# Optimization experiments

Measured on AMD Instinct MI355X. Metric: run time of the kernel, lower is better.

Reference implementation:

```python
import jax, jax.numpy as jnp
import numpy as np

B, T, E, C = 64, 512, 768, 20


def setup_inputs() -> dict:
    key = jax.random.key(0)
    ks = jax.random.split(key, 8)
    hidden = jax.random.normal(ks[0], (B, T, E), jnp.float32)
    attention_mask = jnp.ones((B, T), jnp.int32)
    labels = jax.random.randint(ks[1], (B, T), 0, C)
    fc_w = jax.random.normal(ks[2], (C, E), jnp.float32) * 0.02
    fc_b = jnp.zeros((C,), jnp.float32)
    # torchcrf initializes transitions ~ Uniform(-0.1, 0.1)
    start_transitions = jax.random.uniform(ks[3], (C,), jnp.float32, -0.1, 0.1)
    end_transitions = jax.random.uniform(ks[4], (C,), jnp.float32, -0.1, 0.1)
    transitions = jax.random.uniform(ks[5], (C, C), jnp.float32, -0.1, 0.1)
    return {"hidden": hidden, "attention_mask": attention_mask, "labels": labels,
            "fc_w": fc_w, "fc_b": fc_b, "start_transitions": start_transitions,
            "end_transitions": end_transitions, "transitions": transitions}


def _crf_log_likelihood(emissions, tags, mask, start_t, end_t, trans):
    # emissions [B,T,C], tags [B,T] int, mask [B,T]
    Bn = emissions.shape[0]
    emT = jnp.swapaxes(emissions, 0, 1)            # [T,B,C]
    tagsT = jnp.swapaxes(tags, 0, 1)               # [T,B]
    maskT = jnp.swapaxes(mask, 0, 1).astype(emissions.dtype)  # [T,B]
    barange = jnp.arange(Bn)
    # --- numerator: score of the gold path ---
    score = start_t[tagsT[0]] + emT[0, barange, tagsT[0]]
    def num_step(s, x):
        em_t, tag_t, tag_p, m_t = x
        s = s + (trans[tag_p, tag_t] + em_t[barange, tag_t]) * m_t
        return s, None
    score, _ = jax.lax.scan(num_step, score, (emT[1:], tagsT[1:], tagsT[:-1], maskT[1:]))
    seq_ends = jnp.sum(mask, axis=1).astype(jnp.int32) - 1
    last_tags = tags[barange, seq_ends]
    score = score + end_t[last_tags]
    # --- denominator: forward algorithm (logsumexp recurrence) ---
    alpha = start_t[None, :] + emT[0]              # [B,C]
    def den_step(a, x):
        em_t, m_t = x
        nxt = jax.nn.logsumexp(a[:, :, None] + trans[None, :, :] + em_t[:, None, :], axis=1)
        a = jnp.where(m_t[:, None] > 0, nxt, a)
        return a, None
    alpha, _ = jax.lax.scan(den_step, alpha, (emT[1:], maskT[1:]))
    norm = jax.nn.logsumexp(alpha + end_t[None, :], axis=1)
    return score - norm


def _viterbi_decode(emissions, mask, start_t, end_t, trans):
    emT = jnp.swapaxes(emissions, 0, 1)            # [T,B,C]
    maskT = jnp.swapaxes(mask, 0, 1)               # [T,B]
    alpha = start_t[None, :] + emT[0]              # [B,C]
    def step(a, x):
        em_t, m_t = x
        sc = a[:, :, None] + trans[None, :, :]     # [B, prev C, cur C]
        best = jnp.max(sc, axis=1) + em_t
        idx = jnp.argmax(sc, axis=1)               # [B,C] best prev tag
        a2 = jnp.where(m_t[:, None] > 0, best, a)
        return a2, idx
    alpha, hist = jax.lax.scan(step, alpha, (emT[1:], maskT[1:]))  # hist [T-1,B,C]
    last = jnp.argmax(alpha + end_t[None, :], axis=1)  # [B]
    def back(tag, idx_t):
        prev = jnp.take_along_axis(idx_t, tag[:, None], axis=1)[:, 0]
        return prev, prev
    _, prevs = jax.lax.scan(back, last, hist, reverse=True)  # [T-1,B]
    path = jnp.concatenate([jnp.swapaxes(prevs, 0, 1), last[:, None]], axis=1)  # [B,T]
    return path


def reference(hidden, attention_mask, labels, fc_w, fc_b, start_transitions, end_transitions, transitions):
    # linear head on BERT hidden states -> per-token emissions
    emissions = jnp.einsum('bte,ce->btc', hidden, fc_w) + fc_b
    llh = _crf_log_likelihood(emissions, labels, attention_mask,
                              start_transitions, end_transitions, transitions)
    loss = -jnp.mean(llh)  # crf(..., reduction='mean') negated
    path = _viterbi_decode(emissions, attention_mask, start_transitions,
                           end_transitions, transitions) + 1  # res_paths = x + 1
    return (loss, path)
```

## Files before the change

### kernel.cpp

```cpp
#include <hip/hip_runtime.h>
#include <hip/hip_bf16.h>

#define BB 64
#define TT 512
#define EE 768
#define CC 20
#define MID 256

typedef __attribute__((ext_vector_type(8))) short bf16x8;
typedef __attribute__((ext_vector_type(4))) float f32x4;

__device__ __forceinline__ float rlane(float x, int l) {
  return __int_as_float(__builtin_amdgcn_readlane(__float_as_int(x), l));
}
__device__ __forceinline__ short f2bf(float x) {
  union { __hip_bfloat16 h; short s; } u;
  u.h = __float2bfloat16(x);
  return u.s;
}
__device__ __forceinline__ bf16x8 pack8(float4 a, float4 b) {
  bf16x8 r;
  r[0] = f2bf(a.x); r[1] = f2bf(a.y); r[2] = f2bf(a.z); r[3] = f2bf(a.w);
  r[4] = f2bf(b.x); r[5] = f2bf(b.y); r[6] = f2bf(b.z); r[7] = f2bf(b.w);
  return r;
}

__global__ __launch_bounds__(256) void packw_kernel(const float* __restrict__ fc_w,
                                                    short* __restrict__ wfrag) {
  int t = blockIdx.x * 256 + threadIdx.x;
  int lane = t & 63;
  int kc = (t >> 6) % 24;
  int tile = t / (24 * 64);
  int n = tile * 16 + (lane & 15);
  if (n >= CC) n = CC - 1;
  int k0 = kc * 32 + (lane >> 4) * 8;
  const float* src = fc_w + (size_t)n * EE + k0;
  float4 x = *(const float4*)src;
  float4 y = *(const float4*)(src + 4);
  ((bf16x8*)wfrag)[t] = pack8(x, y);
}

__global__ __launch_bounds__(256) void emissions_kernel(
    const float* __restrict__ hidden, const short* __restrict__ wfrag,
    const float* __restrict__ fc_b, float* __restrict__ em) {
  const int wave = threadIdx.x >> 6;
  const int lane = threadIdx.x & 63;
  const int token0 = blockIdx.x * 64 + wave * 16;
  const int m = lane & 15, q = lane >> 4;
  const float* hrow = hidden + (size_t)(token0 + m) * EE + q * 8;
  const bf16x8* wp = (const bf16x8*)wfrag;
  f32x4 acc0 = {0.f, 0.f, 0.f, 0.f}, acc1 = {0.f, 0.f, 0.f, 0.f};
#pragma unroll 4
  for (int kb = 0; kb < 24; ++kb) {
    float4 a0 = *(const float4*)(hrow + kb * 32);
    float4 a1 = *(const float4*)(hrow + kb * 32 + 4);
    bf16x8 Ab = pack8(a0, a1);
    bf16x8 w0 = wp[kb * 64 + lane];
    bf16x8 w1 = wp[(24 + kb) * 64 + lane];
    acc0 = __builtin_amdgcn_mfma_f32_16x16x32_bf16(Ab, w0, acc0, 0, 0, 0);
    acc1 = __builtin_amdgcn_mfma_f32_16x16x32_bf16(Ab, w1, acc1, 0, 0, 0);
  }
  const int col = lane & 15;
  const float b0v = fc_b[col];
  const bool has1 = (16 + col < CC);
  const float b1v = has1 ? fc_b[16 + col] : 0.f;
#pragma unroll
  for (int r = 0; r < 4; ++r) {
    int tok = token0 + q * 4 + r;
    em[(size_t)tok * CC + col] = acc0[r] + b0v;
    if (has1) em[(size_t)tok * CC + 16 + col] = acc1[r] + b1v;
  }
}

__device__ __forceinline__ unsigned umax_(unsigned a, unsigned b) { return a > b ? a : b; }
__device__ __forceinline__ unsigned umax3_(unsigned a, unsigned b, unsigned c) {
  return umax_(umax_(a, b), c);
}
#define PDECL(Q) unsigned p##Q = (__float_as_uint(rlane(a, Q) + tv[Q]) & 0xFFFFFFE0u) | Q##u;
__device__ __forceinline__ void vstep(float a, const float (&tv)[CC], float& vm, int& jm) {
  PDECL(0) PDECL(1) PDECL(2) PDECL(3) PDECL(4) PDECL(5) PDECL(6) PDECL(7)
  PDECL(8) PDECL(9) PDECL(10) PDECL(11) PDECL(12) PDECL(13) PDECL(14)
  PDECL(15) PDECL(16) PDECL(17) PDECL(18) PDECL(19)
  unsigned m0 = umax3_(p0, p1, p2);
  unsigned m1 = umax3_(p3, p4, p5);
  unsigned m2 = umax3_(p6, p7, p8);
  unsigned m3 = umax3_(p9, p10, p11);
  unsigned m4 = umax3_(p12, p13, p14);
  unsigned m5 = umax3_(p15, p16, p17);
  unsigned n0 = umax3_(m0, m1, m2);
  unsigned n1 = umax3_(m3, m4, m5);
  unsigned n2 = umax_(p18, p19);
  unsigned r = umax3_(n0, n1, n2);
  vm = __uint_as_float(r & 0xFFFFFFE0u);
  jm = (int)(r & 31u);
}

#define XDECL(Q) float x##Q = rlane(x, Q); int y##Q = Q;
#define MRX(A_, B_) { bool k_ = (x##A_ >= x##B_); x##A_ = k_ ? x##A_ : x##B_; y##A_ = k_ ? y##A_ : y##B_; }
__device__ __forceinline__ int lane_argmax(float x) {
  XDECL(0) XDECL(1) XDECL(2) XDECL(3) XDECL(4) XDECL(5) XDECL(6) XDECL(7)
  XDECL(8) XDECL(9) XDECL(10) XDECL(11) XDECL(12) XDECL(13) XDECL(14)
  XDECL(15) XDECL(16) XDECL(17) XDECL(18) XDECL(19)
  MRX(0, 10) MRX(1, 11) MRX(2, 12) MRX(3, 13) MRX(4, 14)
  MRX(5, 15) MRX(6, 16) MRX(7, 17) MRX(8, 18) MRX(9, 19)
  MRX(0, 5) MRX(1, 6) MRX(2, 7) MRX(3, 8) MRX(4, 9)
  MRX(0, 1) MRX(2, 3)
  MRX(0, 2) MRX(0, 4)
  return y0;
}

__device__ __forceinline__ float fdot(float Es, const float (&ET)[CC]) {
  float s0 = rlane(Es, 0) * ET[0];
  float s1 = rlane(Es, 1) * ET[1];
  float s2 = rlane(Es, 2) * ET[2];
  float s3 = rlane(Es, 3) * ET[3];
  s0 = fmaf(rlane(Es, 4), ET[4], s0);
  s1 = fmaf(rlane(Es, 5), ET[5], s1);
  s2 = fmaf(rlane(Es, 6), ET[6], s2);
  s3 = fmaf(rlane(Es, 7), ET[7], s3);
  s0 = fmaf(rlane(Es, 8), ET[8], s0);
  s1 = fmaf(rlane(Es, 9), ET[9], s1);
  s2 = fmaf(rlane(Es, 10), ET[10], s2);
  s3 = fmaf(rlane(Es, 11), ET[11], s3);
  s0 = fmaf(rlane(Es, 12), ET[12], s0);
  s1 = fmaf(rlane(Es, 13), ET[13], s1);
  s2 = fmaf(rlane(Es, 14), ET[14], s2);
  s3 = fmaf(rlane(Es, 15), ET[15], s3);
  s0 = fmaf(rlane(Es, 16), ET[16], s0);
  s1 = fmaf(rlane(Es, 17), ET[17], s1);
  s2 = fmaf(rlane(Es, 18), ET[18], s2);
  s3 = fmaf(rlane(Es, 19), ET[19], s3);
  return (s0 + s1) + (s2 + s3);
}

__global__ __launch_bounds__(64) void crf_half_kernel(
    const float* __restrict__ em, const int* __restrict__ mask,
    const float* __restrict__ st, const float* __restrict__ en,
    const float* __restrict__ tr,
    float* __restrict__ amw, float* __restrict__ bmw,
    float* __restrict__ avw, float* __restrict__ bvw,
    unsigned char* __restrict__ bpws, unsigned char* __restrict__ fpws) {
  __shared__ float emsh[(MID + 1) * CC];
  __shared__ int msh[TT];
  const int tid = threadIdx.x;
  const int quad = blockIdx.x >> 6;
  const int b = blockIdx.x & (BB - 1);
  const int back = quad & 1;
  const int cc = tid < CC ? tid : CC - 1;
  const float K = 1.44269504088896340736f;
  const float BIAS = 64.0f;

  {
    const float* base = em + (size_t)b * TT * CC + (back ? MID * CC : 0);
    int nf4 = back ? (MID * CC / 4) : ((MID + 1) * CC / 4);
    const float4* src = (const float4*)base;
    float4* dst = (float4*)emsh;
    for (int i = tid; i < nf4; i += 64) dst[i] = src[i];
    for (int i = tid; i < TT; i += 64) msh[i] = mask[b * TT + i];
  }
  __syncthreads();

  if (quad == 0) {
    float ET[CC];
#pragma unroll
    for (int q = 0; q < CC; ++q) ET[q] = __builtin_amdgcn_exp2f(tr[q * CC + cc] * K);
    float r = st[cc] + emsh[cc];
    float base0 = rlane(r, 0);
    float Es = __builtin_amdgcn_exp2f((r - base0) * K);
    float off = base0 * K;
    int ie = 0;
    float emc = emsh[CC + cc];
    int mcur = msh[1];
    float eec = __builtin_amdgcn_exp2f(emc * K);
    for (int t = 1; t <= MID; ++t) {
      int tn = (t < MID) ? t + 1 : t;
      float emn = emsh[tn * CC + cc];
      int mn = msh[tn];
      float s = fdot(Es, ET) * eec;
      Es = mcur ? s : Es;
      if ((t & 7) == 0) {
        float p = rlane(Es, 0);
        int e = ((__float_as_int(p) >> 23) & 255) - 127;
        Es *= __int_as_float((127 - e) << 23);
        ie += e;
      }
      eec = __builtin_amdgcn_exp2f(emn * K);
      mcur = mn;
    }
    if (tid < CC) amw[b * CC + tid] = off + (float)ie + __builtin_amdgcn_logf(Es);
  } else if (quad == 1) {
    float ETr[CC];
#pragma unroll
    for (int q = 0; q < CC; ++q) ETr[q] = __builtin_amdgcn_exp2f(tr[cc * CC + q] * K);
    const float ENc = __builtin_amdgcn_exp2f(en[cc] * K);
    float Bs = ENc;
    int ie = 0;
    float em1 = emsh[(TT - 1 - MID) * CC + cc];
    int m1 = msh[TT - 1];
    float ee1 = __builtin_amdgcn_exp2f(em1 * K);
    for (int t = TT - 2; t >= MID; --t) {
      float emn = emsh[(t - MID) * CC + cc];
      int mn = msh[t];
      float G = Bs * ee1;
      float s = fdot(G, ETr);
      Bs = m1 ? s : ENc;
      ie = m1 ? ie : 0;
      if ((t & 7) == 0) {
        float p = rlane(Bs, 0);
        int e = ((__float_as_int(p) >> 23) & 255) - 127;
        Bs *= __int_as_float((127 - e) << 23);
        ie += e;
      }
      ee1 = __builtin_amdgcn_exp2f(emn * K);
      m1 = mn;
    }
    if (tid < CC) bmw[b * CC + tid] = (float)ie + __builtin_amdgcn_logf(Bs);
  } else if (quad == 2) {
    float tv[CC];
#pragma unroll
    for (int q = 0; q < CC; ++q) tv[q] = tr[q * CC + cc];
    float a = st[cc] + emsh[cc] + BIAS;
    float emc = emsh[CC + cc];
    int mcur = msh[1];
    unsigned char* bp = bpws + (size_t)b * MID * CC;
    for (int t = 1; t <= MID; ++t) {
      int tn = (t < MID) ? t + 1 : t;
      float emn = emsh[tn * CC + cc];
      int mn = msh[tn];
      float vm;
      int jm;
      vstep(a, tv, vm, jm);
      if (tid < CC) bp[(t - 1) * CC + tid] = (unsigned char)jm;
      float au = vm + emc;
      a = mcur ? au : a;
      if ((t & 7) == 0) a += (BIAS - rlane(a, 0));
      emc = emn;
      mcur = mn;
    }
    if (tid < CC) avw[b * CC + tid] = a;
  } else {
    float tv[CC];
#pragma unroll
    for (int q = 0; q < CC; ++q) tv[q] = tr[cc * CC + q];
    const float ENv = en[cc] + BIAS;
    float Vb = ENv;
    float em1 = emsh[(TT - 1 - MID) * CC + cc];
    int m1 = msh[TT - 1];
    unsigned char* fp = fpws + (size_t)b * MID * CC;
    for (int t = TT - 2; t >= MID; --t) {
      float emn = emsh[(t - MID) * CC + cc];
      int mn = msh[t];
      float a = Vb + em1;
      float vm;
      int jm;
      vstep(a, tv, vm, jm);
      if (tid < CC) fp[(t - MID) * CC + tid] = (unsigned char)jm;
      Vb = m1 ? vm : ENv;
      if ((t & 7) == 0) Vb += (BIAS - rlane(Vb, 0));
      em1 = emn;
      m1 = mn;
    }
    if (tid < CC) bvw[b * CC + tid] = Vb;
  }
}

__global__ __launch_bounds__(64) void finish_kernel(
    const float* __restrict__ em, const int* __restrict__ mask,
    const int* __restrict__ labels, const float* __restrict__ st,
    const float* __restrict__ en, const float* __restrict__ tr,
    const float* __restrict__ amw, const float* __restrict__ bmw,
    const float* __restrict__ avw, const float* __restrict__ bvw,
    const unsigned char* __restrict__ bpws, const unsigned char* __restrict__ fpws,
    float* __restrict__ llh, float* __restrict__ out) {
  __shared__ unsigned char hl[2 * MID * CC];
  const int b = blockIdx.x;
  const int tid = threadIdx.x;
  const int cc = tid < CC ? tid : CC - 1;
  const float LN2 = 0.69314718055994530942f;
  {
    const int4* bsrc = (const int4*)(bpws + (size_t)b * MID * CC);
    const int4* fsrc = (const int4*)(fpws + (size_t)b * MID * CC);
    int4* dst = (int4*)hl;
    for (int i = tid; i < 320; i += 64) {
      dst[i] = bsrc[i];
      dst[320 + i] = fsrc[i];
    }
  }
  __syncthreads();

  int cstar = lane_argmax(avw[b * CC + cc] + bvw[b * CC + cc]);
  float* ob = out + 1 + (size_t)b * TT;
  if (tid == 0) ob[MID] = (float)(cstar + 1);
  {
    int tag = cstar;
    int s = MID - 1;
    while (s >= 7) {
      int g0 = hl[(s - 0) * CC + cc];
      int g1 = hl[(s - 1) * CC + cc];
      int g2 = hl[(s - 2) * CC + cc];
      int g3 = hl[(s - 3) * CC + cc];
      int g4 = hl[(s - 4) * CC + cc];
      int g5 = hl[(s - 5) * CC + cc];
      int g6 = hl[(s - 6) * CC + cc];
      int g7 = hl[(s - 7) * CC + cc];
      tag = __builtin_amdgcn_readlane(g0, tag); float f0 = (float)(tag + 1);
      tag = __builtin_amdgcn_readlane(g1, tag); float f1 = (float)(tag + 1);
      tag = __builtin_amdgcn_readlane(g2, tag); float f2 = (float)(tag + 1);
      tag = __builtin_amdgcn_readlane(g3, tag); float f3 = (float)(tag + 1);
      tag = __builtin_amdgcn_readlane(g4, tag); float f4 = (float)(tag + 1);
      tag = __builtin_amdgcn_readlane(g5, tag); float f5 = (float)(tag + 1);
      tag = __builtin_amdgcn_readlane(g6, tag); float f6 = (float)(tag + 1);
      tag = __builtin_amdgcn_readlane(g7, tag); float f7 = (float)(tag + 1);
      if (tid == 0) {
        ob[s - 0] = f0; ob[s - 1] = f1; ob[s - 2] = f2; ob[s - 3] = f3;
        ob[s - 4] = f4; ob[s - 5] = f5; ob[s - 6] = f6; ob[s - 7] = f7;
      }
      s -= 8;
    }
  }
  {
    int tag = cstar;
    int u = 0;
    while (u + 7 <= MID - 2) {
      int g0 = hl[MID * CC + (u + 0) * CC + cc];
      int g1 = hl[MID * CC + (u + 1) * CC + cc];
      int g2 = hl[MID * CC + (u + 2) * CC + cc];
      int g3 = hl[MID * CC + (u + 3) * CC + cc];
      int g4 = hl[MID * CC + (u + 4) * CC + cc];
      int g5 = hl[MID * CC + (u + 5) * CC + cc];
      int g6 = hl[MID * CC + (u + 6) * CC + cc];
      int g7 = hl[MID * CC + (u + 7) * CC + cc];
      tag = __builtin_amdgcn_readlane(g0, tag); float f0 = (float)(tag + 1);
      tag = __builtin_amdgcn_readlane(g1, tag); float f1 = (float)(tag + 1);
      tag = __builtin_amdgcn_readlane(g2, tag); float f2 = (float)(tag + 1);
      tag = __builtin_amdgcn_readlane(g3, tag); float f3 = (float)(tag + 1);
      tag = __builtin_amdgcn_readlane(g4, tag); float f4 = (float)(tag + 1);
      tag = __builtin_amdgcn_readlane(g5, tag); float f5 = (float)(tag + 1);
      tag = __builtin_amdgcn_readlane(g6, tag); float f6 = (float)(tag + 1);
      tag = __builtin_amdgcn_readlane(g7, tag); float f7 = (float)(tag + 1);
      if (tid == 0) {
        ob[MID + 1 + u + 0] = f0; ob[MID + 1 + u + 1] = f1;
        ob[MID + 1 + u + 2] = f2; ob[MID + 1 + u + 3] = f3;
        ob[MID + 1 + u + 4] = f4; ob[MID + 1 + u + 5] = f5;
        ob[MID + 1 + u + 6] = f6; ob[MID + 1 + u + 7] = f7;
      }
      u += 8;
    }
    while (u <= MID - 2) {
      int g = hl[MID * CC + u * CC + cc];
      tag = __builtin_amdgcn_readlane(g, tag);
      if (tid == 0) ob[MID + 1 + u] = (float)(tag + 1);
      ++u;
    }
  }

  float zn = amw[b * CC + cc] + bmw[b * CC + cc];
  float M = zn;
#pragma unroll
  for (int o = 32; o >= 1; o >>= 1) M = fmaxf(M, __shfl_xor(M, o));
  float sE = (tid < CC) ? __builtin_amdgcn_exp2f(zn - M) : 0.f;
#pragma unroll
  for (int o = 32; o >= 1; o >>= 1) sE += __shfl_xor(sE, o);
  float norm = LN2 * (M + __builtin_amdgcn_logf(sE));

  const int* lab = labels + b * TT;
  const float* emg = em + (size_t)b * TT * CC;
  float sc = 0.f;
  int msum = 0;
  for (int k = tid; k < TT; k += 64) {
    int mk = mask[b * TT + k];
    msum += mk;
    if (k >= 1) {
      int tg = lab[k], tp = lab[k - 1];
      sc += (tr[tp * CC + tg] + emg[k * CC + tg]) * (float)mk;
    }
  }
#pragma unroll
  for (int o = 32; o >= 1; o >>= 1) {
    sc += __shfl_xor(sc, o);
    msum += __shfl_xor(msum, o);
  }
  int seq_end = msum - 1;
  int t0 = lab[0], tl = lab[seq_end];
  float score = sc + st[t0] + emg[t0] + en[tl];
  if (tid == 0) llh[b] = score - norm;
}

__global__ __launch_bounds__(64) void loss_kernel(const float* __restrict__ llh,
                                                  float* __restrict__ out) {
  float v = llh[threadIdx.x];
#pragma unroll
  for (int o = 32; o >= 1; o >>= 1) v += __shfl_xor(v, o);
  if (threadIdx.x == 0) out[0] = -(v * (1.0f / 64.0f));
}

extern "C" void kernel_launch(void* const* d_in, const int* in_sizes, int n_in,
                              void* d_out, int out_size, void* d_ws, size_t ws_size,
                              hipStream_t stream) {
  const float* hidden = (const float*)d_in[0];
  const int* amask = (const int*)d_in[1];
  const int* labels = (const int*)d_in[2];
  const float* fc_w = (const float*)d_in[3];
  const float* fc_b = (const float*)d_in[4];
  const float* st = (const float*)d_in[5];
  const float* en = (const float*)d_in[6];
  const float* tr = (const float*)d_in[7];

  float* emws = (float*)d_ws;
  float* llh = emws + (size_t)BB * TT * CC;
  short* wfrag = (short*)(llh + 64);
  float* amw = (float*)(wfrag + 24576);
  float* bmw = amw + BB * CC;
  float* avw = bmw + BB * CC;
  float* bvw = avw + BB * CC;
  unsigned char* bpws = (unsigned char*)(bvw + BB * CC);
  unsigned char* fpws = bpws + (size_t)BB * MID * CC;
  float* out = (float*)d_out;

  packw_kernel<<<(2 * 24 * 64) / 256, 256, 0, stream>>>(fc_w, wfrag);
  emissions_kernel<<<(BB * TT) / 64, 256, 0, stream>>>(hidden, wfrag, fc_b, emws);
  crf_half_kernel<<<4 * BB, 64, 0, stream>>>(emws, amask, st, en, tr,
                                             amw, bmw, avw, bvw, bpws, fpws);
  finish_kernel<<<BB, 64, 0, stream>>>(emws, amask, labels, st, en, tr,
                                       amw, bmw, avw, bvw, bpws, fpws, llh, out);
  loss_kernel<<<1, 64, 0, stream>>>(llh, out);
}
```

Baseline: 250.5 us.

## Interleave four batch rows per CRF wave and fold loss reduction into atomics

Each CRF workgroup now runs the forward, backward and Viterbi recurrences for four batch rows at once. The four independent dependency chains interleave and hide the latency of readlane and exp, at the cost of fewer workgroups (64 instead of 256). The shared-memory staging of emissions and mask is dropped, so each step reads global memory directly. The separate loss kernel is removed: the output is zeroed in the weight-pack kernel and finish_kernel accumulates the mean loss with atomicAdd, which saves one launch but makes the summation order nondeterministic.

```diff
diff --git a/kernel.cpp b/kernel.cpp
--- a/kernel.cpp
+++ b/kernel.cpp
@@ -6,6 +6,7 @@
 #define EE 768
 #define CC 20
 #define MID 256
+#define NB 4
 
 typedef __attribute__((ext_vector_type(8))) short bf16x8;
 typedef __attribute__((ext_vector_type(4))) float f32x4;
@@ -26,7 +27,9 @@
 }
 
 __global__ __launch_bounds__(256) void packw_kernel(const float* __restrict__ fc_w,
-                                                    short* __restrict__ wfrag) {
+                                                    short* __restrict__ wfrag,
+                                                    float* __restrict__ outp) {
+  if (blockIdx.x == 0 && threadIdx.x == 0) outp[0] = 0.f;
   int t = blockIdx.x * 256 + threadIdx.x;
   int lane = t & 63;
   int kc = (t >> 6) % 24;
@@ -76,11 +79,12 @@
 __device__ __forceinline__ unsigned umax3_(unsigned a, unsigned b, unsigned c) {
   return umax_(umax_(a, b), c);
 }
-#define PDECL(Q) unsigned p##Q = (__float_as_uint(rlane(a, Q) + tv[Q]) & 0xFFFFFFE0u) | Q##u;
 __device__ __forceinline__ void vstep(float a, const float (&tv)[CC], float& vm, int& jm) {
-  PDECL(0) PDECL(1) PDECL(2) PDECL(3) PDECL(4) PDECL(5) PDECL(6) PDECL(7)
-  PDECL(8) PDECL(9) PDECL(10) PDECL(11) PDECL(12) PDECL(13) PDECL(14)
-  PDECL(15) PDECL(16) PDECL(17) PDECL(18) PDECL(19)
+#define PKEY(Q) unsigned p##Q = (__float_as_uint(rlane(a, Q) + tv[Q]) & 0xFFFFFFE0u) | Q##u;
+  PKEY(0) PKEY(1) PKEY(2) PKEY(3) PKEY(4) PKEY(5) PKEY(6) PKEY(7)
+  PKEY(8) PKEY(9) PKEY(10) PKEY(11) PKEY(12) PKEY(13) PKEY(14)
+  PKEY(15) PKEY(16) PKEY(17) PKEY(18) PKEY(19)
+#undef PKEY
   unsigned m0 = umax3_(p0, p1, p2);
   unsigned m1 = umax3_(p3, p4, p5);
   unsigned m2 = umax3_(p6, p7, p8);
@@ -133,6 +137,14 @@
   return (s0 + s1) + (s2 + s3);
 }
 
+#define RENORM(Xs, iev)                                        \
+  {                                                            \
+    float p_ = rlane(Xs, 0);                                   \
+    int e_ = ((__float_as_int(p_) >> 23) & 255) - 127;         \
+    Xs *= __int_as_float((127 - e_) << 23);                    \
+    iev += e_;                                                 \
+  }
+
 __global__ __launch_bounds__(64) void crf_half_kernel(
     const float* __restrict__ em, const int* __restrict__ mask,
     const float* __restrict__ st, const float* __restrict__ en,
@@ -140,127 +152,180 @@
     float* __restrict__ amw, float* __restrict__ bmw,
     float* __restrict__ avw, float* __restrict__ bvw,
     unsigned char* __restrict__ bpws, unsigned char* __restrict__ fpws) {
-  __shared__ float emsh[(MID + 1) * CC];
-  __shared__ int msh[TT];
   const int tid = threadIdx.x;
-  const int quad = blockIdx.x >> 6;
-  const int b = blockIdx.x & (BB - 1);
-  const int back = quad & 1;
+  const int quad = blockIdx.x >> 4;
+  const int b0 = (blockIdx.x & 15) * NB;
   const int cc = tid < CC ? tid : CC - 1;
   const float K = 1.44269504088896340736f;
   const float BIAS = 64.0f;
-
-  {
-    const float* base = em + (size_t)b * TT * CC + (back ? MID * CC : 0);
-    int nf4 = back ? (MID * CC / 4) : ((MID + 1) * CC / 4);
-    const float4* src = (const float4*)base;
-    float4* dst = (float4*)emsh;
-    for (int i = tid; i < nf4; i += 64) dst[i] = src[i];
-    for (int i = tid; i < TT; i += 64) msh[i] = mask[b * TT + i];
-  }
-  __syncthreads();
+  const float* eb = em + (size_t)b0 * TT * CC;
+  const int* mb = mask + b0 * TT;
 
   if (quad == 0) {
     float ET[CC];
 #pragma unroll
     for (int q = 0; q < CC; ++q) ET[q] = __builtin_amdgcn_exp2f(tr[q * CC + cc] * K);
-    float r = st[cc] + emsh[cc];
-    float base0 = rlane(r, 0);
-    float Es = __builtin_amdgcn_exp2f((r - base0) * K);
-    float off = base0 * K;
-    int ie = 0;
-    float emc = emsh[CC + cc];
-    int mcur = msh[1];
-    float eec = __builtin_amdgcn_exp2f(emc * K);
+    float Es[NB], off[NB], eec[NB];
+    int ie[NB], mcur[NB];
+#pragma unroll
+    for (int i = 0; i < NB; ++i) {
+      float r = st[cc] + eb[i * TT * CC + cc];
+      float bv = rlane(r, 0);
+      Es[i] = __builtin_amdgcn_exp2f((r - bv) * K);
+      off[i] = bv * K;
+      ie[i] = 0;
+      eec[i] = __builtin_amdgcn_exp2f(eb[i * TT * CC + CC + cc] * K);
+      mcur[i] = mb[i * TT + 1];
+    }
     for (int t = 1; t <= MID; ++t) {
       int tn = (t < MID) ? t + 1 : t;
-      float emn = emsh[tn * CC + cc];
-      int mn = msh[tn];
-      float s = fdot(Es, ET) * eec;
-      Es = mcur ? s : Es;
+      float emn[NB]; int mn[NB];
+#pragma unroll
+      for (int i = 0; i < NB; ++i) {
+        emn[i] = eb[i * TT * CC + tn * CC + cc];
+        mn[i] = mb[i * TT + tn];
+      }
+#pragma unroll
+      for (int i = 0; i < NB; ++i) {
+        float s = fdot(Es[i], ET) * eec[i];
+        Es[i] = mcur[i] ? s : Es[i];
+      }
       if ((t & 7) == 0) {
-        float p = rlane(Es, 0);
-        int e = ((__float_as_int(p) >> 23) & 255) - 127;
-        Es *= __int_as_float((127 - e) << 23);
-        ie += e;
-      }
-      eec = __builtin_amdgcn_exp2f(emn * K);
-      mcur = mn;
-    }
-    if (tid < CC) amw[b * CC + tid] = off + (float)ie + __builtin_amdgcn_logf(Es);
+#pragma unroll
+        for (int i = 0; i < NB; ++i) RENORM(Es[i], ie[i])
+      }
+#pragma unroll
+      for (int i = 0; i < NB; ++i) {
+        eec[i] = __builtin_amdgcn_exp2f(emn[i] * K);
+        mcur[i] = mn[i];
+      }
+    }
+    if (tid < CC) {
+#pragma unroll
+      for (int i = 0; i < NB; ++i)
+        amw[(b0 + i) * CC + tid] = off[i] + (float)ie[i] + __builtin_amdgcn_logf(Es[i]);
+    }
   } else if (quad == 1) {
     float ETr[CC];
 #pragma unroll
     for (int q = 0; q < CC; ++q) ETr[q] = __builtin_amdgcn_exp2f(tr[cc * CC + q] * K);
     const float ENc = __builtin_amdgcn_exp2f(en[cc] * K);
-    float Bs = ENc;
-    int ie = 0;
-    float em1 = emsh[(TT - 1 - MID) * CC + cc];
-    int m1 = msh[TT - 1];
-    float ee1 = __builtin_amdgcn_exp2f(em1 * K);
+    float Bs[NB], ee1[NB];
+    int ie[NB], m1[NB];
+#pragma unroll
+    for (int i = 0; i < NB; ++i) {
+      Bs[i] = ENc;
+      ie[i] = 0;
+      ee1[i] = __builtin_amdgcn_exp2f(eb[i * TT * CC + (TT - 1) * CC + cc] * K);
+      m1[i] = mb[i * TT + TT - 1];
+    }
     for (int t = TT - 2; t >= MID; --t) {
-      float emn = emsh[(t - MID) * CC + cc];
-      int mn = msh[t];
-      float G = Bs * ee1;
-      float s = fdot(G, ETr);
-      Bs = m1 ? s : ENc;
-      ie = m1 ? ie : 0;
+      float emn[NB]; int mn[NB];
+#pragma unroll
+      for (int i = 0; i < NB; ++i) {
+        emn[i] = eb[i * TT * CC + t * CC + cc];
+        mn[i] = mb[i * TT + t];
+      }
+#pragma unroll
+      for (int i = 0; i < NB; ++i) {
+        float G = Bs[i] * ee1[i];
+        float s = fdot(G, ETr);
+        Bs[i] = m1[i] ? s : ENc;
+        ie[i] = m1[i] ? ie[i] : 0;
+      }
       if ((t & 7) == 0) {
-        float p = rlane(Bs, 0);
-        int e = ((__float_as_int(p) >> 23) & 255) - 127;
-        Bs *= __int_as_float((127 - e) << 23);
-        ie += e;
-      }
-      ee1 = __builtin_amdgcn_exp2f(emn * K);
-      m1 = mn;
-    }
-    if (tid < CC) bmw[b * CC + tid] = (float)ie + __builtin_amdgcn_logf(Bs);
+#pragma unroll
+        for (int i = 0; i < NB; ++i) RENORM(Bs[i], ie[i])
+      }
+#pragma unroll
+      for (int i = 0; i < NB; ++i) {
+        ee1[i] = __builtin_amdgcn_exp2f(emn[i] * K);
+        m1[i] = mn[i];
+      }
+    }
+    if (tid < CC) {
+#pragma unroll
+      for (int i = 0; i < NB; ++i)
+        bmw[(b0 + i) * CC + tid] = (float)ie[i] + __builtin_amdgcn_logf(Bs[i]);
+    }
   } else if (quad == 2) {
     float tv[CC];
 #pragma unroll
     for (int q = 0; q < CC; ++q) tv[q] = tr[q * CC + cc];
-    float a = st[cc] + emsh[cc] + BIAS;
-    float emc = emsh[CC + cc];
-    int mcur = msh[1];
-    unsigned char* bp = bpws + (size_t)b * MID * CC;
+    float a[NB], emc[NB];
+    int mcur[NB];
+#pragma unroll
+    for (int i = 0; i < NB; ++i) {
+      a[i] = st[cc] + eb[i * TT * CC + cc] + BIAS;
+      emc[i] = eb[i * TT * CC + CC + cc];
+      mcur[i] = mb[i * TT + 1];
+    }
     for (int t = 1; t <= MID; ++t) {
       int tn = (t < MID) ? t + 1 : t;
-      float emn = emsh[tn * CC + cc];
-      int mn = msh[tn];
-      float vm;
-      int jm;
-      vstep(a, tv, vm, jm);
-      if (tid < CC) bp[(t - 1) * CC + tid] = (unsigned char)jm;
-      float au = vm + emc;
-      a = mcur ? au : a;
-      if ((t & 7) == 0) a += (BIAS - rlane(a, 0));
-      emc = emn;
-      mcur = mn;
-    }
-    if (tid < CC) avw[b * CC + tid] = a;
+      float emn[NB]; int mn[NB];
+#pragma unroll
+      for (int i = 0; i < NB; ++i) {
+        emn[i] = eb[i * TT * CC + tn * CC + cc];
+        mn[i] = mb[i * TT + tn];
+      }
+#pragma unroll
+      for (int i = 0; i < NB; ++i) {
+        float vm; int jm;
+        vstep(a[i], tv, vm, jm);
+        if (tid < CC) bpws[(size_t)(b0 + i) * MID * CC + (t - 1) * CC + tid] = (unsigned char)jm;
+        float au = vm + emc[i];
+        a[i] = mcur[i] ? au : a[i];
+      }
+      if ((t & 7) == 0) {
+#pragma unroll
+        for (int i = 0; i < NB; ++i) a[i] += (BIAS - rlane(a[i], 0));
+      }
+#pragma unroll
+      for (int i = 0; i < NB; ++i) { emc[i] = emn[i]; mcur[i] = mn[i]; }
+    }
+    if (tid < CC) {
+#pragma unroll
+      for (int i = 0; i < NB; ++i) avw[(b0 + i) * CC + tid] = a[i];
+    }
   } else {
     float tv[CC];
 #pragma unroll
     for (int q = 0; q < CC; ++q) tv[q] = tr[cc * CC + q];
     const float ENv = en[cc] + BIAS;
-    float Vb = ENv;
-    float em1 = emsh[(TT - 1 - MID) * CC + cc];
-    int m1 = msh[TT - 1];
-    unsigned char* fp = fpws + (size_t)b * MID * CC;
+    float Vb[NB], em1[NB];
+    int m1[NB];
+#pragma unroll
+    for (int i = 0; i < NB; ++i) {
+      Vb[i] = ENv;
+      em1[i] = eb[i * TT * CC + (TT - 1) * CC + cc];
+      m1[i] = mb[i * TT + TT - 1];
+    }
     for (int t = TT - 2; t >= MID; --t) {
-      float emn = emsh[(t - MID) * CC + cc];
-      int mn = msh[t];
-      float a = Vb + em1;
-      float vm;
-      int jm;
-      vstep(a, tv, vm, jm);
-      if (tid < CC) fp[(t - MID) * CC + tid] = (unsigned char)jm;
-      Vb = m1 ? vm : ENv;
-      if ((t & 7) == 0) Vb += (BIAS - rlane(Vb, 0));
-      em1 = emn;
-      m1 = mn;
-    }
-    if (tid < CC) bvw[b * CC + tid] = Vb;
+      float emn[NB]; int mn[NB];
+#pragma unroll
+      for (int i = 0; i < NB; ++i) {
+        emn[i] = eb[i * TT * CC + t * CC + cc];
+        mn[i] = mb[i * TT + t];
+      }
+#pragma unroll
+      for (int i = 0; i < NB; ++i) {
+        float av = Vb[i] + em1[i];
+        float vm; int jm;
+        vstep(av, tv, vm, jm);
+        if (tid < CC) fpws[(size_t)(b0 + i) * MID * CC + (t - MID) * CC + tid] = (unsigned char)jm;
+        Vb[i] = m1[i] ? vm : ENv;
+      }
+      if ((t & 7) == 0) {
+#pragma unroll
+        for (int i = 0; i < NB; ++i) Vb[i] += (BIAS - rlane(Vb[i], 0));
+      }
+#pragma unroll
+      for (int i = 0; i < NB; ++i) { em1[i] = emn[i]; m1[i] = mn[i]; }
+    }
+    if (tid < CC) {
+#pragma unroll
+      for (int i = 0; i < NB; ++i) bvw[(b0 + i) * CC + tid] = Vb[i];
+    }
   }
 }
 
@@ -271,7 +336,7 @@
     const float* __restrict__ amw, const float* __restrict__ bmw,
     const float* __restrict__ avw, const float* __restrict__ bvw,
     const unsigned char* __restrict__ bpws, const unsigned char* __restrict__ fpws,
-    float* __restrict__ llh, float* __restrict__ out) {
+    float* __restrict__ out) {
   __shared__ unsigned char hl[2 * MID * CC];
   const int b = blockIdx.x;
   const int tid = threadIdx.x;
@@ -383,15 +448,7 @@
   int seq_end = msum - 1;
   int t0 = lab[0], tl = lab[seq_end];
   float score = sc + st[t0] + emg[t0] + en[tl];
-  if (tid == 0) llh[b] = score - norm;
-}
-
-__global__ __launch_bounds__(64) void loss_kernel(const float* __restrict__ llh,
-                                                  float* __restrict__ out) {
-  float v = llh[threadIdx.x];
-#pragma unroll
-  for (int o = 32; o >= 1; o >>= 1) v += __shfl_xor(v, o);
-  if (threadIdx.x == 0) out[0] = -(v * (1.0f / 64.0f));
+  if (tid == 0) atomicAdd(out, (norm - score) * (1.0f / 64.0f));
 }
 
 extern "C" void kernel_launch(void* const* d_in, const int* in_sizes, int n_in,
@@ -417,11 +474,10 @@
   unsigned char* fpws = bpws + (size_t)BB * MID * CC;
   float* out = (float*)d_out;
 
-  packw_kernel<<<(2 * 24 * 64) / 256, 256, 0, stream>>>(fc_w, wfrag);
+  packw_kernel<<<(2 * 24 * 64) / 256, 256, 0, stream>>>(fc_w, wfrag, out);
   emissions_kernel<<<(BB * TT) / 64, 256, 0, stream>>>(hidden, wfrag, fc_b, emws);
-  crf_half_kernel<<<4 * BB, 64, 0, stream>>>(emws, amask, st, en, tr,
-                                             amw, bmw, avw, bvw, bpws, fpws);
+  crf_half_kernel<<<4 * (BB / NB), 64, 0, stream>>>(emws, amask, st, en, tr,
+                                                    amw, bmw, avw, bvw, bpws, fpws);
   finish_kernel<<<BB, 64, 0, stream>>>(emws, amask, labels, st, en, tr,
-                                       amw, bmw, avw, bvw, bpws, fpws, llh, out);
-  loss_kernel<<<1, 64, 0, stream>>>(llh, out);
-}
+                                       amw, bmw, avw, bvw, bpws, fpws, out);
+}
```

New measurement: 398.7 us. 59.1% more time.
